# Optimization experiments

Hardware: AMD Instinct MI355X
Metric: run time of the kernel (lower is better)

## Reference

```python
import jax, jax.numpy as jnp
import numpy as np

# Config mirrors TACO_hashed init: data_size=[1024,1024], dimensions=[[4]*5,[4]*5]
N = 262144          # number of query coordinates
DH = 256            # dim_hidden
TD = 4              # tile_dim = dimensions[0][0]
NLEV = 5            # n_levels
W0C = 30.0          # w0
DIMS = np.array([[4]*NLEV, [4]*NLEV])                 # [2, n_levels]
CUM = 1024 // np.cumprod(DIMS, axis=1)                # cum_bases per axis, [2, n_levels]


def setup_inputs() -> dict:
    key = jax.random.key(0)
    ks = jax.random.split(key, 9)
    s = 1.0 / np.sqrt(DH)
    e = TD * TD  # embedding dim = tile_dim**2 = 16
    return {
        "coords": jax.random.randint(ks[0], (N, 2), 0, 1024, dtype=jnp.int32),
        "W0": jax.random.normal(ks[1], (2, DH), jnp.float32) * (1.0 / np.sqrt(2.0)),
        "b0": jnp.zeros((DH,), jnp.float32),
        "Wh": jax.random.normal(ks[2], (3, DH, DH), jnp.float32) * s,  # hidden SIREN linears
        "bh": jnp.zeros((3, DH), jnp.float32),
        "emb": jax.random.normal(ks[3], (NLEV - 1, e, e), jnp.float32),      # per-level embedding tables
        "modW": jax.random.normal(ks[4], (NLEV - 1, e, DH), jnp.float32) * (1.0 / np.sqrt(e)),  # modulator linears (no bias)
        "Wl": jax.random.normal(ks[5], (DH, 3), jnp.float32) * s,  # last_layer
        "bl": jnp.zeros((3,), jnp.float32),
    }


def reference(coords, W0, b0, Wh, bh, emb, modW, Wl, bl):
    dims = jnp.asarray(DIMS.T)   # [n_levels, 2]
    cum = jnp.asarray(CUM.T)     # [n_levels, 2]
    # decompose_coords: per-level bitwise-style div/mod  -> [N, n_levels, 2]
    lv = (coords[:, None, :] // cum[None]) % dims[None]
    # modulator indices for levels 1..n_levels-1: idx = y*tile_dim + x  -> [N, n_levels-1]
    idx = lv[:, 1:, 1] * TD + lv[:, 1:, 0]
    # SIREN input is level-0 coords as float (faithful to the source)
    x = lv[:, 0, :].astype(jnp.float32) @ W0 + b0
    x = x + W0C * (emb[0][idx[:, 0]] @ modW[0])
    x = jnp.sin(W0C * x)
    for j in range(3):
        x = x @ Wh[j] + bh[j]
        x = x + W0C * (emb[j + 1][idx[:, j + 1]] @ modW[j + 1])
        x = jnp.sin(W0C * x)
    return x @ Wl + bl
```

## Files before the change

### kernel.cpp

```cpp
#include <hip/hip_runtime.h>
#include <hip/hip_bf16.h>
#include <math.h>


typedef float  f32x4  __attribute__((ext_vector_type(4)));
typedef int    i32x4  __attribute__((ext_vector_type(4)));
typedef __bf16 bf16x8 __attribute__((ext_vector_type(8)));

__device__ __forceinline__ float fbar(float v) {
  asm volatile("" : "+v"(v));
  return v;
}

__device__ __forceinline__ unsigned short f2bf_rne(float x) {
  unsigned u = __float_as_uint(x);
  unsigned r = (u + 0x7fffu + ((u >> 16) & 1u)) >> 16;
  return (unsigned short)r;
}

__device__ __forceinline__ float sin30(float x) {
  const float Ch = 4.774648189544678f;
  const float Cl = 1.0321218e-07f;
  float revh = x * Ch;
  fbar(revh);
  float e    = __builtin_fmaf(x, Ch, -revh);
  float revl = __builtin_fmaf(x, Cl, e);
  float k2   = __builtin_rintf(revh + revh);
  float g    = __builtin_fmaf(k2, -0.5f, revh) + revl;
  float g2 = g * g;
  float r = -15.0946f;
  r = __builtin_fmaf(r, g2, 42.0601f);
  r = __builtin_fmaf(r, g2, -76.70585f);
  r = __builtin_fmaf(r, g2, 81.6052492f);
  r = __builtin_fmaf(r, g2, -41.341702f);
  r = __builtin_fmaf(r, g2, 6.2831853f);
  float s = g * r;
  int ki = (int)k2;
  return __uint_as_float(__float_as_uint(s) ^ ((unsigned)(ki & 1) << 31));
}

__device__ __forceinline__ void sincos30(float x, float* so, float* co) {
  const float Ch = 4.774648189544678f;
  const float Cl = 1.0321218e-07f;
  float revh = x * Ch;
  fbar(revh);
  float e    = __builtin_fmaf(x, Ch, -revh);
  float revl = __builtin_fmaf(x, Cl, e);
  float k2   = __builtin_rintf(revh + revh);
  float g    = __builtin_fmaf(k2, -0.5f, revh) + revl;
  float u = g * g;
  float sr = -15.0946f;
  sr = __builtin_fmaf(sr, u, 42.0601f);
  sr = __builtin_fmaf(sr, u, -76.70585f);
  sr = __builtin_fmaf(sr, u, 81.6052492f);
  sr = __builtin_fmaf(sr, u, -41.341702f);
  sr = __builtin_fmaf(sr, u, 6.2831853f);
  float s = g * sr;
  float cr = -26.4259f;
  cr = __builtin_fmaf(cr, u, 60.2446f);
  cr = __builtin_fmaf(cr, u, -85.4568f);
  cr = __builtin_fmaf(cr, u, 64.9393940f);
  cr = __builtin_fmaf(cr, u, -19.7392088f);
  float c = __builtin_fmaf(cr, u, 1.0f);
  int ki = (int)k2;
  unsigned sgn = ((unsigned)(ki & 1)) << 31;
  *so = __uint_as_float(__float_as_uint(s) ^ sgn);
  *co = __uint_as_float(__float_as_uint(c) ^ sgn);
}

__global__ void k_prep(const float* __restrict__ emb, const float* __restrict__ modW,
                       float* __restrict__ Mf, const float* __restrict__ W2,
                       unsigned short* __restrict__ B2T) {
  int b = blockIdx.x, d = threadIdx.x;
  if (b < 64) {
    int j = b >> 4, i = b & 15;
    float acc = 0.0f;
#pragma unroll
    for (int e = 0; e < 16; ++e)
      acc = __builtin_fmaf(emb[j * 256 + i * 16 + e], modW[(j * 16 + e) * 256 + d], acc);
    Mf[b * 256 + d] = acc;
  } else {
    int col = b - 64, k = d;
    float w = W2[k * 256 + col];
    unsigned short hi = f2bf_rne(w);
    float hif = __uint_as_float((unsigned)hi << 16);
    unsigned short lo = f2bf_rne(w - hif);
    B2T[col * 768 + k] = hi;
    B2T[col * 768 + 256 + k] = lo;
    B2T[col * 768 + 512 + k] = hi;
  }
}

__global__ void k_prep2(const float* __restrict__ Mf3, const float* __restrict__ Wl,
                        unsigned* __restrict__ B2u) {
  int col = blockIdx.x, d = threadIdx.x;
  int i3 = col / 3, q = col - 3 * (col / 3);
  float pm = fbar(30.0f * Mf3[i3 * 256 + d]);
  float s, c;
  sincos30(pm, &s, &c);
  float w = Wl[d * 3 + q];
  unsigned ts = (unsigned)f2bf_rne(s * w);
  unsigned tc = (unsigned)f2bf_rne(c * w);
  B2u[col * 256 + d] = (tc << 16) | ts;
}

__global__ void __launch_bounds__(256) k_h123(
    const float* __restrict__ W0, const float* __restrict__ b0,
    const float* __restrict__ Wh0, const float* __restrict__ bh0,
    const float* __restrict__ W1, const float* __restrict__ b1,
    const float* __restrict__ Mf,
    unsigned short* __restrict__ Ah, unsigned short* __restrict__ Al) {
  __shared__ float xs1[256];
  __shared__ float xs2[4][256];
  int b = blockIdx.x, d = threadIdx.x;
  int c1 = b >> 2;
  float lvx = (float)((c1 >> 6) & 3), lvy = (float)((c1 >> 4) & 3);
  int i0 = c1 & 15;
  float t = fbar(lvx * W0[d]);
  t = __builtin_fmaf(lvy, W0[256 + d], t);
  t = fbar(t + b0[d]);
  float p = fbar(30.0f * Mf[i0 * 256 + d]);
  float xv = fbar(t + p);
  xs1[d] = sinf(fbar(30.0f * xv));
  __syncthreads();
  float acc = 0.0f;
  for (int k = 0; k < 256; ++k)
    acc = __builtin_fmaf(xs1[k], Wh0[k * 256 + d], acc);
  float t2 = fbar(acc + bh0[d]);
#pragma unroll
  for (int r = 0; r < 4; ++r) {
    int i1 = 4 * (b & 3) + r;
    float pp = fbar(30.0f * Mf[4096 + i1 * 256 + d]);
    float x2 = fbar(t2 + pp);
    xs2[r][d] = sinf(fbar(30.0f * x2));
  }
  __syncthreads();
  float m2[16];
#pragma unroll
  for (int i = 0; i < 16; ++i) m2[i] = fbar(30.0f * Mf[8192 + i * 256 + d]);
  float acc3[4];
#pragma unroll
  for (int r = 0; r < 4; ++r) acc3[r] = 0.0f;
  for (int k = 0; k < 256; ++k) {
    float w = W1[k * 256 + d];
#pragma unroll
    for (int r = 0; r < 4; ++r) acc3[r] = __builtin_fmaf(xs2[r][k], w, acc3[r]);
  }
  float bias = b1[d];
#pragma unroll
  for (int r = 0; r < 4; ++r) {
    float tr = fbar(acc3[r] + bias);
    int c3base = (b * 4 + r) * 16;
#pragma unroll
    for (int i = 0; i < 16; ++i) {
      float x = fbar(tr + m2[i]);
      float h = sin30(x);
      unsigned short hi = f2bf_rne(h);
      float hif = __uint_as_float((unsigned)hi << 16);
      unsigned short lo = f2bf_rne(h - hif);
      size_t o = (size_t)(c3base + i) * 256 + d;
      Ah[o] = hi;
      Al[o] = lo;
    }
  }
}

__global__ void __launch_bounds__(512, 1) k_gemm(
    const unsigned short* __restrict__ Ah, const unsigned short* __restrict__ Al,
    const unsigned short* __restrict__ B2T, const float* __restrict__ b2,
    unsigned* __restrict__ SC) {
  __shared__ unsigned short As[128 * 40];
  __shared__ unsigned short Bs[256 * 40];
  const int t = threadIdx.x;
  const int lane = t & 63, wid = t >> 6;
  const int l15 = lane & 15, l4 = lane >> 4;
  const int wm = (wid >> 2) * 64;
  const int wn = (wid & 3) * 64;
  const size_t r0 = (size_t)blockIdx.x * 128;

  const int s_arow = t >> 2, s_apart = t & 3;
  const int s_bcol0 = t >> 2, s_bcol1 = 128 + (t >> 2), s_bpart = t & 3;

  f32x4 acc[4][4];
#pragma unroll
  for (int rf = 0; rf < 4; ++rf)
#pragma unroll
    for (int cf = 0; cf < 4; ++cf) acc[rf][cf] = (f32x4){0.f, 0.f, 0.f, 0.f};

  i32x4 ra, rb0, rb1;
  ra  = *(const i32x4*)(Ah + ((r0 + s_arow) << 8) + s_apart * 8);
  rb0 = *(const i32x4*)(B2T + s_bcol0 * 768 + s_bpart * 8);
  rb1 = *(const i32x4*)(B2T + s_bcol1 * 768 + s_bpart * 8);

#pragma unroll 1
  for (int c = 0; c < 24; ++c) {
    *(i32x4*)(As + s_arow * 40 + s_apart * 8) = ra;
    *(i32x4*)(Bs + s_bcol0 * 40 + s_bpart * 8) = rb0;
    *(i32x4*)(Bs + s_bcol1 * 40 + s_bpart * 8) = rb1;
    __syncthreads();
    if (c < 23) {
      int cn = c + 1;
      int kk = cn & 7;
      const unsigned short* asrc = (cn >= 16) ? Al : Ah;
      ra  = *(const i32x4*)(asrc + ((r0 + s_arow) << 8) + kk * 32 + s_apart * 8);
      rb0 = *(const i32x4*)(B2T + s_bcol0 * 768 + cn * 32 + s_bpart * 8);
      rb1 = *(const i32x4*)(B2T + s_bcol1 * 768 + cn * 32 + s_bpart * 8);
    }
    bf16x8 af[4], bfr[4];
#pragma unroll
    for (int rf = 0; rf < 4; ++rf)
      af[rf] = __builtin_bit_cast(
          bf16x8, *(const i32x4*)(As + (wm + rf * 16 + l15) * 40 + l4 * 8));
#pragma unroll
    for (int cf = 0; cf < 4; ++cf)
      bfr[cf] = __builtin_bit_cast(
          bf16x8, *(const i32x4*)(Bs + (wn + cf * 16 + l15) * 40 + l4 * 8));
#pragma unroll
    for (int rf = 0; rf < 4; ++rf)
#pragma unroll
      for (int cf = 0; cf < 4; ++cf)
        acc[rf][cf] = __builtin_amdgcn_mfma_f32_16x16x32_bf16(
            af[rf], bfr[cf], acc[rf][cf], 0, 0, 0);
    __syncthreads();
  }

#pragma unroll
  for (int cf = 0; cf < 4; ++cf) {
    float bias = b2[wn + cf * 16 + l15];
#pragma unroll
    for (int rf = 0; rf < 4; ++rf) {
      size_t rbase = r0 + wm + rf * 16 + l4 * 4;
#pragma unroll
      for (int j = 0; j < 4; ++j) {
        float g = acc[rf][cf][j] + bias;
        float s, c;
        sincos30(g, &s, &c);
        unsigned pk = ((unsigned)f2bf_rne(s) << 16) | (unsigned)f2bf_rne(c);
        SC[(rbase + j) * 256 + wn + cf * 16 + l15] = pk;
      }
    }
  }
}

__global__ void __launch_bounds__(512, 1) k_ugemm(
    const unsigned short* __restrict__ SCb, const unsigned* __restrict__ B2u,
    float* __restrict__ U) {
  __shared__ unsigned short As[128 * 40];
  __shared__ unsigned Bs[48 * 260];
  const int t = threadIdx.x;
  const int lane = t & 63, wid = t >> 6;
  const int l15 = lane & 15, l4 = lane >> 4;
  const int wm = wid * 16;
  const size_t r0 = (size_t)blockIdx.x * 128;

#pragma unroll
  for (int i = 0; i < 24; ++i) {
    int lin = t + i * 512;
    int col = lin >> 8, kp = lin & 255;
    Bs[col * 260 + kp] = B2u[lin];
  }

  const int s_row = t >> 2, s_part = t & 3;
  f32x4 acc[3];
#pragma unroll
  for (int cf = 0; cf < 3; ++cf) acc[cf] = (f32x4){0.f, 0.f, 0.f, 0.f};

  i32x4 ra = *(const i32x4*)(SCb + (r0 + s_row) * 512 + s_part * 8);
#pragma unroll 1
  for (int c = 0; c < 16; ++c) {
    *(i32x4*)(As + s_row * 40 + s_part * 8) = ra;
    __syncthreads();
    if (c < 15)
      ra = *(const i32x4*)(SCb + (r0 + s_row) * 512 + (c + 1) * 32 + s_part * 8);
    bf16x8 af = __builtin_bit_cast(
        bf16x8, *(const i32x4*)(As + (wm + l15) * 40 + l4 * 8));
#pragma unroll
    for (int cf = 0; cf < 3; ++cf) {
      bf16x8 bfr = __builtin_bit_cast(
          bf16x8, *(const i32x4*)(Bs + (cf * 16 + l15) * 260 + c * 16 + l4 * 4));
      acc[cf] = __builtin_amdgcn_mfma_f32_16x16x32_bf16(af, bfr, acc[cf], 0, 0, 0);
    }
    __syncthreads();
  }

#pragma unroll
  for (int cf = 0; cf < 3; ++cf) {
    size_t rbase = r0 + wm + l4 * 4;
#pragma unroll
    for (int j = 0; j < 4; ++j)
      U[(rbase + j) * 48 + cf * 16 + l15] = acc[cf][j];
  }
}

__global__ void k_gather(const int* __restrict__ coords, const float* __restrict__ U,
                         const float* __restrict__ bl, float* __restrict__ out, int N) {
  int n = blockIdx.x * blockDim.x + threadIdx.x;
  if (n >= N) return;
  int x = coords[2 * n], y = coords[2 * n + 1];
  int c1 = ((x >> 8) & 3) * 64 + ((y >> 8) & 3) * 16 +
           (((y >> 6) & 3) * 4 + ((x >> 6) & 3));
  int i1 = ((y >> 4) & 3) * 4 + ((x >> 4) & 3);
  int i2 = ((y >> 2) & 3) * 4 + ((x >> 2) & 3);
  int i3 = (y & 3) * 4 + (x & 3);
  int c3 = (c1 * 16 + i1) * 16 + i2;
  const float* up = U + (size_t)c3 * 48 + i3 * 3;
  out[n * 3 + 0] = up[0] + bl[0];
  out[n * 3 + 1] = up[1] + bl[1];
  out[n * 3 + 2] = up[2] + bl[2];
}

__global__ void k_direct(const int* __restrict__ coords, const float* __restrict__ W0,
                         const float* __restrict__ b0, const float* __restrict__ Wh,
                         const float* __restrict__ bh, const float* __restrict__ emb,
                         const float* __restrict__ modW, const float* __restrict__ Wl,
                         const float* __restrict__ bl, float* __restrict__ out) {
  __shared__ float xs[256];
  __shared__ float red[256];
  int n = blockIdx.x, d = threadIdx.x;
  int x = coords[2 * n], y = coords[2 * n + 1];
  float lvx = (float)((x >> 8) & 3), lvy = (float)((y >> 8) & 3);
  int idx[4];
  idx[0] = ((y >> 6) & 3) * 4 + ((x >> 6) & 3);
  idx[1] = ((y >> 4) & 3) * 4 + ((x >> 4) & 3);
  idx[2] = ((y >> 2) & 3) * 4 + ((x >> 2) & 3);
  idx[3] = (y & 3) * 4 + (x & 3);
  float m = 0.0f;
#pragma unroll
  for (int e = 0; e < 16; ++e)
    m = __builtin_fmaf(emb[idx[0] * 16 + e], modW[e * 256 + d], m);
  float t = fbar(lvx * W0[d]);
  t = __builtin_fmaf(lvy, W0[256 + d], t);
  t = fbar(t + b0[d]);
  float p = fbar(30.0f * m);
  float xv = fbar(t + p);
  xs[d] = sinf(fbar(30.0f * xv));
  __syncthreads();
  for (int j = 0; j < 3; ++j) {
    float acc = 0.0f;
    for (int k = 0; k < 256; ++k)
      acc = __builtin_fmaf(xs[k], Wh[j * 65536 + k * 256 + d], acc);
    float tt = fbar(acc + bh[j * 256 + d]);
    m = 0.0f;
#pragma unroll
    for (int e = 0; e < 16; ++e)
      m = __builtin_fmaf(emb[(j + 1) * 256 + idx[j + 1] * 16 + e],
                         modW[((j + 1) * 16 + e) * 256 + d], m);
    p = fbar(30.0f * m);
    xv = fbar(tt + p);
    float h = sinf(fbar(30.0f * xv));
    __syncthreads();
    xs[d] = h;
    __syncthreads();
  }
  for (int q = 0; q < 3; ++q) {
    red[d] = xs[d] * Wl[d * 3 + q];
    __syncthreads();
    for (int s = 128; s > 0; s >>= 1) {
      if (d < s) red[d] += red[d + s];
      __syncthreads();
    }
    if (d == 0) out[n * 3 + q] = red[0] + bl[q];
    __syncthreads();
  }
}

extern "C" void kernel_launch(void* const* d_in, const int* in_sizes, int n_in,
                              void* d_out, int out_size, void* d_ws, size_t ws_size,
                              hipStream_t stream) {
  const int*   coords = (const int*)d_in[0];
  const float* W0   = (const float*)d_in[1];
  const float* b0   = (const float*)d_in[2];
  const float* Wh   = (const float*)d_in[3];
  const float* bh   = (const float*)d_in[4];
  const float* emb  = (const float*)d_in[5];
  const float* modW = (const float*)d_in[6];
  const float* Wl   = (const float*)d_in[7];
  const float* bl   = (const float*)d_in[8];
  float* out = (float*)d_out;
  const int N = in_sizes[0] / 2;

  const size_t OFF_MF  = 0;
  const size_t OFF_B2T = 65536;
  const size_t OFF_AH  = 458752;
  const size_t OFF_AL  = 34013184;
  const size_t OFF_SC  = 67567616;
  const size_t OFF_B2  = 134676480;
  const size_t OFF_U   = OFF_AH;
  const size_t NEED    = 134774784;

  if (ws_size >= NEED) {
    char* ws = (char*)d_ws;
    float*          Mf  = (float*)(ws + OFF_MF);
    unsigned short* B2T = (unsigned short*)(ws + OFF_B2T);
    unsigned short* Ahp = (unsigned short*)(ws + OFF_AH);
    unsigned short* Alp = (unsigned short*)(ws + OFF_AL);
    unsigned*       SC  = (unsigned*)(ws + OFF_SC);
    unsigned*       B2u = (unsigned*)(ws + OFF_B2);
    float*          U   = (float*)(ws + OFF_U);

    k_prep<<<320, 256, 0, stream>>>(emb, modW, Mf, Wh + 131072, B2T);
    k_prep2<<<48, 256, 0, stream>>>(Mf + 12288, Wl, B2u);
    k_h123<<<1024, 256, 0, stream>>>(W0, b0, Wh, bh, Wh + 65536, bh + 256, Mf,
                                     Ahp, Alp);
    k_gemm<<<512, 512, 0, stream>>>(Ahp, Alp, B2T, bh + 512, SC);
    k_ugemm<<<512, 512, 0, stream>>>((const unsigned short*)SC, B2u, U);
    k_gather<<<(N + 255) / 256, 256, 0, stream>>>(coords, U, bl, out, N);
  } else {
    k_direct<<<N, 256, 0, stream>>>(coords, W0, b0, Wh, bh, emb, modW, Wl, bl, out);
  }
}
```

Before: 113.1 us.

## Merge prep kernels, use sin-addition identity, and double-buffer GEMM via direct LDS loads

Folds k_prep2 into k_prep, which removes one launch. k_h123 now computes sin(30(t+m)) through the angle-addition identity, using per-level cos/sin tables built once, so it replaces 64 polynomial sin evaluations per thread with 4 sincos calls plus FMAs. The k_gemm main loop switches from register-staged copies into a padded LDS tile to global_load_lds asynchronous loads into a double-buffered, unpadded LDS tile, so the next k-chunk loads while the current one computes. The risks are that the trig identity changes rounding, the unpadded LDS layout may cause bank conflicts, and the only barrier per iteration comes after the MFMAs with no explicit wait on the async loads.

```diff
diff --git a/kernel.cpp b/kernel.cpp
--- a/kernel.cpp
+++ b/kernel.cpp
@@ -18,25 +18,10 @@
   return (unsigned short)r;
 }
 
-__device__ __forceinline__ float sin30(float x) {
-  const float Ch = 4.774648189544678f;
-  const float Cl = 1.0321218e-07f;
-  float revh = x * Ch;
-  fbar(revh);
-  float e    = __builtin_fmaf(x, Ch, -revh);
-  float revl = __builtin_fmaf(x, Cl, e);
-  float k2   = __builtin_rintf(revh + revh);
-  float g    = __builtin_fmaf(k2, -0.5f, revh) + revl;
-  float g2 = g * g;
-  float r = -15.0946f;
-  r = __builtin_fmaf(r, g2, 42.0601f);
-  r = __builtin_fmaf(r, g2, -76.70585f);
-  r = __builtin_fmaf(r, g2, 81.6052492f);
-  r = __builtin_fmaf(r, g2, -41.341702f);
-  r = __builtin_fmaf(r, g2, 6.2831853f);
-  float s = g * r;
-  int ki = (int)k2;
-  return __uint_as_float(__float_as_uint(s) ^ ((unsigned)(ki & 1) << 31));
+__device__ __forceinline__ void gload16(const void* g, void* l) {
+  __builtin_amdgcn_global_load_lds(
+      (const __attribute__((address_space(1))) unsigned*)g,
+      (__attribute__((address_space(3))) unsigned*)l, 16, 0, 0);
 }
 
 __device__ __forceinline__ void sincos30(float x, float* so, float* co) {
@@ -69,7 +54,9 @@
 }
 
 __global__ void k_prep(const float* __restrict__ emb, const float* __restrict__ modW,
-                       float* __restrict__ Mf, const float* __restrict__ W2,
+                       float* __restrict__ Mf, float* __restrict__ T2C,
+                       float* __restrict__ T2S, const float* __restrict__ Wl,
+                       unsigned* __restrict__ B2u, const float* __restrict__ W2,
                        unsigned short* __restrict__ B2T) {
   int b = blockIdx.x, d = threadIdx.x;
   if (b < 64) {
@@ -79,6 +66,24 @@
     for (int e = 0; e < 16; ++e)
       acc = __builtin_fmaf(emb[j * 256 + i * 16 + e], modW[(j * 16 + e) * 256 + d], acc);
     Mf[b * 256 + d] = acc;
+    if (j == 2) {
+      float pm = fbar(30.0f * acc);
+      float s, c;
+      sincos30(pm, &s, &c);
+      T2C[i * 256 + d] = c;
+      T2S[i * 256 + d] = s;
+    } else if (j == 3) {
+      float pm = fbar(30.0f * acc);
+      float s, c;
+      sincos30(pm, &s, &c);
+#pragma unroll
+      for (int q = 0; q < 3; ++q) {
+        float w = Wl[d * 3 + q];
+        unsigned ts = (unsigned)f2bf_rne(s * w);
+        unsigned tc = (unsigned)f2bf_rne(c * w);
+        B2u[(i * 3 + q) * 256 + d] = (tc << 16) | ts;
+      }
+    }
   } else {
     int col = b - 64, k = d;
     float w = W2[k * 256 + col];
@@ -91,24 +96,12 @@
   }
 }
 
-__global__ void k_prep2(const float* __restrict__ Mf3, const float* __restrict__ Wl,
-                        unsigned* __restrict__ B2u) {
-  int col = blockIdx.x, d = threadIdx.x;
-  int i3 = col / 3, q = col - 3 * (col / 3);
-  float pm = fbar(30.0f * Mf3[i3 * 256 + d]);
-  float s, c;
-  sincos30(pm, &s, &c);
-  float w = Wl[d * 3 + q];
-  unsigned ts = (unsigned)f2bf_rne(s * w);
-  unsigned tc = (unsigned)f2bf_rne(c * w);
-  B2u[col * 256 + d] = (tc << 16) | ts;
-}
-
 __global__ void __launch_bounds__(256) k_h123(
     const float* __restrict__ W0, const float* __restrict__ b0,
     const float* __restrict__ Wh0, const float* __restrict__ bh0,
     const float* __restrict__ W1, const float* __restrict__ b1,
-    const float* __restrict__ Mf,
+    const float* __restrict__ Mf, const float* __restrict__ T2C,
+    const float* __restrict__ T2S,
     unsigned short* __restrict__ Ah, unsigned short* __restrict__ Al) {
   __shared__ float xs1[256];
   __shared__ float xs2[4][256];
@@ -135,26 +128,28 @@
     xs2[r][d] = sinf(fbar(30.0f * x2));
   }
   __syncthreads();
-  float m2[16];
-#pragma unroll
-  for (int i = 0; i < 16; ++i) m2[i] = fbar(30.0f * Mf[8192 + i * 256 + d]);
-  float acc3[4];
-#pragma unroll
-  for (int r = 0; r < 4; ++r) acc3[r] = 0.0f;
+  float acc3[4] = {0.f, 0.f, 0.f, 0.f};
   for (int k = 0; k < 256; ++k) {
     float w = W1[k * 256 + d];
 #pragma unroll
     for (int r = 0; r < 4; ++r) acc3[r] = __builtin_fmaf(xs2[r][k], w, acc3[r]);
   }
+  float tcv[16], tsv[16];
+#pragma unroll
+  for (int i = 0; i < 16; ++i) {
+    tcv[i] = T2C[i * 256 + d];
+    tsv[i] = T2S[i * 256 + d];
+  }
   float bias = b1[d];
 #pragma unroll
   for (int r = 0; r < 4; ++r) {
-    float tr = fbar(acc3[r] + bias);
+    float targ = fbar(acc3[r] + bias);
+    float sT, cT;
+    sincos30(targ, &sT, &cT);
     int c3base = (b * 4 + r) * 16;
 #pragma unroll
     for (int i = 0; i < 16; ++i) {
-      float x = fbar(tr + m2[i]);
-      float h = sin30(x);
+      float h = __builtin_fmaf(cT, tsv[i], sT * tcv[i]);
       unsigned short hi = f2bf_rne(h);
       float hif = __uint_as_float((unsigned)hi << 16);
       unsigned short lo = f2bf_rne(h - hif);
@@ -169,8 +164,8 @@
     const unsigned short* __restrict__ Ah, const unsigned short* __restrict__ Al,
     const unsigned short* __restrict__ B2T, const float* __restrict__ b2,
     unsigned* __restrict__ SC) {
-  __shared__ unsigned short As[128 * 40];
-  __shared__ unsigned short Bs[256 * 40];
+  __shared__ unsigned short As[2][128 * 32];
+  __shared__ unsigned short Bs[2][256 * 32];
   const int t = threadIdx.x;
   const int lane = t & 63, wid = t >> 6;
   const int l15 = lane & 15, l4 = lane >> 4;
@@ -178,8 +173,8 @@
   const int wn = (wid & 3) * 64;
   const size_t r0 = (size_t)blockIdx.x * 128;
 
-  const int s_arow = t >> 2, s_apart = t & 3;
-  const int s_bcol0 = t >> 2, s_bcol1 = 128 + (t >> 2), s_bpart = t & 3;
+  const int arow = t >> 2, apart = t & 3;
+  const size_t bcol0 = t >> 2, bcol1 = (t >> 2) + 128;
 
   f32x4 acc[4][4];
 #pragma unroll
@@ -187,34 +182,32 @@
 #pragma unroll
     for (int cf = 0; cf < 4; ++cf) acc[rf][cf] = (f32x4){0.f, 0.f, 0.f, 0.f};
 
-  i32x4 ra, rb0, rb1;
-  ra  = *(const i32x4*)(Ah + ((r0 + s_arow) << 8) + s_apart * 8);
-  rb0 = *(const i32x4*)(B2T + s_bcol0 * 768 + s_bpart * 8);
-  rb1 = *(const i32x4*)(B2T + s_bcol1 * 768 + s_bpart * 8);
-
+#define STAGE(c, bb)                                                         \
+  {                                                                          \
+    const unsigned short* asrc = ((c) >= 16) ? Al : Ah;                      \
+    gload16(asrc + ((r0 + arow) << 8) + ((c) & 7) * 32 + apart * 8,          \
+            (void*)(&As[bb][wid * 512]));                                    \
+    gload16(B2T + bcol0 * 768 + (c) * 32 + apart * 8,                        \
+            (void*)(&Bs[bb][wid * 512]));                                    \
+    gload16(B2T + bcol1 * 768 + (c) * 32 + apart * 8,                        \
+            (void*)(&Bs[bb][(wid + 8) * 512]));                              \
+  }
+
+  STAGE(0, 0);
+  __syncthreads();
 #pragma unroll 1
   for (int c = 0; c < 24; ++c) {
-    *(i32x4*)(As + s_arow * 40 + s_apart * 8) = ra;
-    *(i32x4*)(Bs + s_bcol0 * 40 + s_bpart * 8) = rb0;
-    *(i32x4*)(Bs + s_bcol1 * 40 + s_bpart * 8) = rb1;
-    __syncthreads();
-    if (c < 23) {
-      int cn = c + 1;
-      int kk = cn & 7;
-      const unsigned short* asrc = (cn >= 16) ? Al : Ah;
-      ra  = *(const i32x4*)(asrc + ((r0 + s_arow) << 8) + kk * 32 + s_apart * 8);
-      rb0 = *(const i32x4*)(B2T + s_bcol0 * 768 + cn * 32 + s_bpart * 8);
-      rb1 = *(const i32x4*)(B2T + s_bcol1 * 768 + cn * 32 + s_bpart * 8);
-    }
+    int cur = c & 1;
+    if (c < 23) STAGE(c + 1, cur ^ 1);
     bf16x8 af[4], bfr[4];
 #pragma unroll
     for (int rf = 0; rf < 4; ++rf)
       af[rf] = __builtin_bit_cast(
-          bf16x8, *(const i32x4*)(As + (wm + rf * 16 + l15) * 40 + l4 * 8));
+          bf16x8, *(const i32x4*)(&As[cur][(wm + rf * 16 + l15) * 32 + l4 * 8]));
 #pragma unroll
     for (int cf = 0; cf < 4; ++cf)
       bfr[cf] = __builtin_bit_cast(
-          bf16x8, *(const i32x4*)(Bs + (wn + cf * 16 + l15) * 40 + l4 * 8));
+          bf16x8, *(const i32x4*)(&Bs[cur][(wn + cf * 16 + l15) * 32 + l4 * 8]));
 #pragma unroll
     for (int rf = 0; rf < 4; ++rf)
 #pragma unroll
@@ -223,6 +216,7 @@
             af[rf], bfr[cf], acc[rf][cf], 0, 0, 0);
     __syncthreads();
   }
+#undef STAGE
 
 #pragma unroll
   for (int cf = 0; cf < 4; ++cf) {
@@ -385,8 +379,10 @@
   const size_t OFF_AL  = 34013184;
   const size_t OFF_SC  = 67567616;
   const size_t OFF_B2  = 134676480;
+  const size_t OFF_T2C = 134774784;
+  const size_t OFF_T2S = 134791168;
   const size_t OFF_U   = OFF_AH;
-  const size_t NEED    = 134774784;
+  const size_t NEED    = 134807552;
 
   if (ws_size >= NEED) {
     char* ws = (char*)d_ws;
@@ -396,12 +392,14 @@
     unsigned short* Alp = (unsigned short*)(ws + OFF_AL);
     unsigned*       SC  = (unsigned*)(ws + OFF_SC);
     unsigned*       B2u = (unsigned*)(ws + OFF_B2);
+    float*          T2C = (float*)(ws + OFF_T2C);
+    float*          T2S = (float*)(ws + OFF_T2S);
     float*          U   = (float*)(ws + OFF_U);
 
-    k_prep<<<320, 256, 0, stream>>>(emb, modW, Mf, Wh + 131072, B2T);
-    k_prep2<<<48, 256, 0, stream>>>(Mf + 12288, Wl, B2u);
+    k_prep<<<320, 256, 0, stream>>>(emb, modW, Mf, T2C, T2S, Wl, B2u,
+                                    Wh + 131072, B2T);
     k_h123<<<1024, 256, 0, stream>>>(W0, b0, Wh, bh, Wh + 65536, bh + 256, Mf,
-                                     Ahp, Alp);
+                                     T2C, T2S, Ahp, Alp);
     k_gemm<<<512, 512, 0, stream>>>(Ahp, Alp, B2T, bh + 512, SC);
     k_ugemm<<<512, 512, 0, stream>>>((const unsigned short*)SC, B2u, U);
     k_gather<<<(N + 255) / 256, 256, 0, stream>>>(coords, U, bl, out, N);
```

Result: faster. 105.4 us (-6.8%).
